# Optimization experiments

Hardware: AMD Instinct MI355X
Metric: run time of the kernel (lower is better)

## Reference

```python
import jax, jax.numpy as jnp
import numpy as np

B, S, E, H = 4, 2048, 1024, 16
D = E // H  # head_size = 64

def setup_inputs() -> dict:
    key = jax.random.key(0)
    ks = jax.random.split(key, 10)
    s_e = E ** -0.5
    s_4e = (4 * E) ** -0.5
    inp = {
        "x": jax.random.normal(ks[0], (B, S, E), dtype=jnp.float32),
        # per-head Q/K/V weights, stacked: [H, E, D], no bias
        "Wq": jax.random.normal(ks[1], (H, E, D), dtype=jnp.float32) * s_e,
        "Wk": jax.random.normal(ks[2], (H, E, D), dtype=jnp.float32) * s_e,
        "Wv": jax.random.normal(ks[3], (H, E, D), dtype=jnp.float32) * s_e,
        "Wo": jax.random.normal(ks[4], (E, E), dtype=jnp.float32) * s_e,
        "bo": jax.random.normal(ks[5], (E,), dtype=jnp.float32) * 0.01,
        "W1": jax.random.normal(ks[6], (E, 4 * E), dtype=jnp.float32) * s_e,
        "b1": jax.random.normal(ks[7], (4 * E,), dtype=jnp.float32) * 0.01,
        "W2": jax.random.normal(ks[8], (4 * E, E), dtype=jnp.float32) * s_4e,
        "b2": jax.random.normal(ks[9], (E,), dtype=jnp.float32) * 0.01,
    }
    return inp

def reference(x, Wq, Wk, Wv, Wo, bo, W1, b1, W2, b2):
    b, s, e = x.shape
    # NOTE: original scales by embedding_size**-0.5 (Size of x), not head_size
    scale = e ** -0.5
    q = jnp.einsum("bse,hed->bhsd", x, Wq)
    k = jnp.einsum("bse,hed->bhsd", x, Wk)
    v = jnp.einsum("bse,hed->bhsd", x, Wv)
    scores = jnp.einsum("bhsd,bhtd->bhst", q, k) * scale
    causal = jnp.tril(jnp.ones((s, s), dtype=bool))
    scores = jnp.where(causal, scores, -jnp.inf)
    weights = jax.nn.softmax(scores, axis=-1)
    attn = jnp.einsum("bhst,bhtd->bhsd", weights, v)  # [B,H,S,D]
    # concat heads along last dim: [B,S,H*D]
    attn = attn.transpose(0, 2, 1, 3).reshape(b, s, e)
    y = attn @ Wo + bo
    x = x + y  # residual (no LayerNorm applied in original forward)
    h = jax.nn.relu(x @ W1 + b1)
    ffn = h @ W2 + b2
    return x + ffn
```

## Files before the change

kernel.cpp:

```cpp
#include <hip/hip_runtime.h>
#include <stdint.h>

#define B_ 4
#define S_ 2048
#define E_ 1024
#define H_ 16
#define D_ 64

typedef unsigned short u16;
typedef u16 u16x8 __attribute__((ext_vector_type(8)));
typedef __bf16 bf16x8 __attribute__((ext_vector_type(8)));
typedef float f32x4 __attribute__((ext_vector_type(4)));

__device__ __forceinline__ float bf2f(u16 x) {
  unsigned int v = ((unsigned int)x) << 16;
  return __builtin_bit_cast(float, v);
}
__device__ __forceinline__ u16 f2bf(float f) {
  unsigned int u = __builtin_bit_cast(unsigned int, f);
  unsigned int r = (u + 0x7fffu + ((u >> 16) & 1u)) >> 16;
  return (u16)r;
}

__device__ __forceinline__ void gl2lds16(const u16* g, u16* l) {
  __builtin_amdgcn_global_load_lds(
      (const __attribute__((address_space(1))) void*)g,
      (__attribute__((address_space(3))) void*)l, 16, 0, 0);
}

__global__ __launch_bounds__(256) void cast_bf16_k(const float* __restrict__ src,
                                                   u16* __restrict__ dst, long n) {
  long i = ((long)blockIdx.x * 256 + threadIdx.x) * 8;
  if (i + 8 <= n) {
    f32x4 a = *(const f32x4*)(src + i), b = *(const f32x4*)(src + i + 4);
    u16x8 o;
#pragma unroll
    for (int j = 0; j < 4; j++) { o[j] = f2bf(a[j]); o[j + 4] = f2bf(b[j]); }
    *(u16x8*)(dst + i) = o;
  }
}

__global__ __launch_bounds__(256) void castT_k(const float* __restrict__ src,
                                               u16* __restrict__ dst, int R, int C) {
  long bofs = (long)blockIdx.z * R * C;
  src += bofs; dst += bofs;
  __shared__ u16 t[32][33];
  int c0 = blockIdx.x * 32, r0 = blockIdx.y * 32;
  int lc = threadIdx.x & 31, lr8 = threadIdx.x >> 5;
#pragma unroll
  for (int i = 0; i < 4; i++) {
    int lr = lr8 + i * 8;
    t[lr][lc] = f2bf(src[(long)(r0 + lr) * C + c0 + lc]);
  }
  __syncthreads();
#pragma unroll
  for (int i = 0; i < 4; i++) {
    int lr = lr8 + i * 8;
    dst[(long)(c0 + lr) * R + r0 + lc] = t[lc][lr];
  }
}

__global__ __launch_bounds__(256) void vT_k(const u16* __restrict__ QKV,
                                            u16* __restrict__ VTg) {
  int bh = blockIdx.z, d0 = blockIdx.y * 32, t0 = blockIdx.x * 32;
  int b = bh >> 4, h = bh & 15;
  __shared__ u16 t[32][33];
  int lc = threadIdx.x & 31, lr8 = threadIdx.x >> 5;
#pragma unroll
  for (int i = 0; i < 4; i++) {
    int lr = lr8 + i * 8;
    t[lr][lc] = QKV[(long)(b * S_ + t0 + lr) * 3072 + 2048 + h * 64 + d0 + lc];
  }
  __syncthreads();
#pragma unroll
  for (int i = 0; i < 4; i++) {
    int lr = lr8 + i * 8;
    VTg[((long)bh * 64 + d0 + lr) * S_ + t0 + lc] = t[lc][lr];
  }
}

template <bool AF32, bool CF32>
__global__ __launch_bounds__(256) void gemm128(const void* __restrict__ Av,
                                               const u16* __restrict__ BT,
                                               void* __restrict__ Cv,
                                               const float* __restrict__ bias,
                                               const float* __restrict__ resid,
                                               int M, int N, int K, int relu,
                                               u16* __restrict__ Cbf) {
  __shared__ u16 As[128 * 32];
  __shared__ u16 Bs[128 * 32];
  const int tid = threadIdx.x;
  const int wave = tid >> 6, lane = tid & 63;
  const int m0 = blockIdx.y * 128, n0 = blockIdx.x * 128;
  const int wm = wave >> 1, wn = wave & 1;
  const int fr = lane & 15, quad = lane >> 4;

  f32x4 acc[4][4] = {};

  const int srow = wave * 32 + (lane >> 2);
  const int skcol = (lane & 3) * 8;

  for (int k0 = 0; k0 < K; k0 += 32) {
    __syncthreads();
    if (AF32) {
      const float* Ap = (const float*)Av + (long)(m0 + (tid >> 1)) * K + k0 + (tid & 1) * 16;
      f32x4 f0 = *(const f32x4*)Ap, f1 = *(const f32x4*)(Ap + 4);
      f32x4 f2 = *(const f32x4*)(Ap + 8), f3 = *(const f32x4*)(Ap + 12);
      u16x8 p0, p1;
#pragma unroll
      for (int j = 0; j < 4; j++) {
        p0[j] = f2bf(f0[j]); p0[j + 4] = f2bf(f1[j]);
        p1[j] = f2bf(f2[j]); p1[j + 4] = f2bf(f3[j]);
      }
      *(u16x8*)&As[(tid >> 1) * 32 + (tid & 1) * 16] = p0;
      *(u16x8*)&As[(tid >> 1) * 32 + (tid & 1) * 16 + 8] = p1;
    } else {
      const u16* Ag = (const u16*)Av + (long)(m0 + srow) * K + k0 + skcol;
      gl2lds16(Ag, &As[(wave * 32) * 32]);
      gl2lds16(Ag + 16 * (long)K, &As[(wave * 32 + 16) * 32]);
    }
    {
      const u16* Bg = BT + (long)(n0 + srow) * K + k0 + skcol;
      gl2lds16(Bg, &Bs[(wave * 32) * 32]);
      gl2lds16(Bg + 16 * (long)K, &Bs[(wave * 32 + 16) * 32]);
    }
    __syncthreads();

    bf16x8 af[4], bfr[4];
#pragma unroll
    for (int mi = 0; mi < 4; mi++)
      af[mi] = __builtin_bit_cast(bf16x8, *(const u16x8*)&As[(wm * 64 + mi * 16 + fr) * 32 + quad * 8]);
#pragma unroll
    for (int ni = 0; ni < 4; ni++)
      bfr[ni] = __builtin_bit_cast(bf16x8, *(const u16x8*)&Bs[(wn * 64 + ni * 16 + fr) * 32 + quad * 8]);
#pragma unroll
    for (int mi = 0; mi < 4; mi++)
#pragma unroll
      for (int ni = 0; ni < 4; ni++)
        acc[mi][ni] = __builtin_amdgcn_mfma_f32_16x16x32_bf16(af[mi], bfr[ni], acc[mi][ni], 0, 0, 0);
  }

#pragma unroll
  for (int mi = 0; mi < 4; mi++)
#pragma unroll
    for (int ni = 0; ni < 4; ni++)
#pragma unroll
      for (int r = 0; r < 4; r++) {
        int gm = m0 + wm * 64 + mi * 16 + quad * 4 + r;
        int gn = n0 + wn * 64 + ni * 16 + fr;
        float v = acc[mi][ni][r];
        if (bias) v += bias[gn];
        if (resid) v += resid[(long)gm * N + gn];
        if (relu) v = fmaxf(v, 0.f);
        if (CF32) ((float*)Cv)[(long)gm * N + gn] = v;
        else      ((u16*)Cv)[(long)gm * N + gn] = f2bf(v);
        if (Cbf) Cbf[(long)gm * N + gn] = f2bf(v);
      }
}

__device__ __forceinline__ bf16x8 ldfrag32(const u16* base, int r, int quad) {
  int u = (r * 32 + quad * 8) ^ (((r >> 3) & 1) << 4);
  return __builtin_bit_cast(bf16x8, *(const u16x8*)(base + u));
}

__device__ __forceinline__ void stage_tile(const u16* __restrict__ A,
                                           const u16* __restrict__ BT, int K,
                                           int m0, int n0, int k0,
                                           u16* __restrict__ buf,
                                           int sr_, int sc_, int wbase) {
#pragma unroll
  for (int h = 0; h < 2; h++) {
    int r = h * 128 + sr_;
    int c = sc_ ^ (((r >> 3) & 1) << 4);
    gl2lds16(A + (size_t)(m0 + r) * K + k0 + c, buf + h * 4096 + wbase);
  }
  int c = sc_ ^ (((sr_ >> 3) & 1) << 4);
  gl2lds16(BT + (size_t)(n0 + sr_) * K + k0 + c, buf + 8192 + wbase);
}

template <bool CF32>
__global__ __launch_bounds__(512) void gemm3b(const u16* __restrict__ A,
                                              const u16* __restrict__ BT,
                                              void* __restrict__ Cv,
                                              const float* __restrict__ bias,
                                              const float* __restrict__ resid,
                                              int M, int N, int K, int relu,
                                              u16* __restrict__ Cbf) {
  (void)M;
  constexpr int BM = 256, BN = 128, BK = 32;
  constexpr int AU = BM * BK;
  constexpr int BUF = AU + BN * BK;

  __shared__ u16 sm[3 * BUF];
  const int tid = threadIdx.x;
  const int wave = tid >> 6, lane = tid & 63;
  const int wm = wave >> 1, wn = wave & 1;
  const int fr = lane & 15, quad = lane >> 4;

  const int nbx = gridDim.x;
  const int nwg = nbx * (int)gridDim.y;
  const int wgid = blockIdx.y * nbx + blockIdx.x;
  const int qq = nwg >> 3, rr = nwg & 7;
  const int xcd = wgid & 7, loc = wgid >> 3;
  const int sw = (xcd < rr ? xcd * (qq + 1) : rr * (qq + 1) + (xcd - rr) * qq) + loc;
  const int n0 = (sw % nbx) * BN;
  const int m0 = (sw / nbx) * BM;

  const int NT = K / BK;

  f32x4 acc[4][4] = {};

  const int sc_ = (tid & 3) * 8;
  const int sr_ = tid >> 2;
  const int wbase = wave << 9;

  const int rA = wm * 64 + fr;
  const int rB = wn * 64 + fr;

  stage_tile(A, BT, K, m0, n0, 0, sm, sr_, sc_, wbase);
  if (NT > 1) {
    stage_tile(A, BT, K, m0, n0, BK, sm + BUF, sr_, sc_, wbase);
    asm volatile("s_waitcnt vmcnt(3)" ::: "memory");
  } else {
    asm volatile("s_waitcnt vmcnt(0)" ::: "memory");
  }
  __builtin_amdgcn_s_barrier();

  int cur = 0;
  for (int t = 0; t < NT; ++t) {
    u16* cb = sm + cur * BUF;

    if (t + 2 < NT) {
      int s2 = cur + 2; if (s2 >= 3) s2 -= 3;
      stage_tile(A, BT, K, m0, n0, (t + 2) * BK, sm + s2 * BUF, sr_, sc_, wbase);
    }

    bf16x8 aF[4], bF[4];
#pragma unroll
    for (int mi = 0; mi < 4; ++mi) aF[mi] = ldfrag32(cb, rA + mi * 16, quad);
#pragma unroll
    for (int ni = 0; ni < 4; ++ni) bF[ni] = ldfrag32(cb + AU, rB + ni * 16, quad);

    asm volatile("s_waitcnt lgkmcnt(0)" ::: "memory");
    __builtin_amdgcn_sched_barrier(0);
    __builtin_amdgcn_s_setprio(1);
#pragma unroll
    for (int mi = 0; mi < 4; ++mi)
#pragma unroll
      for (int ni = 0; ni < 4; ++ni)
        acc[mi][ni] = __builtin_amdgcn_mfma_f32_16x16x32_bf16(aF[mi], bF[ni], acc[mi][ni], 0, 0, 0);
    __builtin_amdgcn_s_setprio(0);

    if (t + 2 < NT) asm volatile("s_waitcnt vmcnt(3)" ::: "memory");
    else            asm volatile("s_waitcnt vmcnt(0)" ::: "memory");
    __builtin_amdgcn_s_barrier();
    cur = cur + 1; if (cur >= 3) cur -= 3;
  }

#pragma unroll
  for (int mi = 0; mi < 4; ++mi)
#pragma unroll
    for (int ni = 0; ni < 4; ++ni)
#pragma unroll
      for (int r = 0; r < 4; ++r) {
        int gm = m0 + wm * 64 + mi * 16 + quad * 4 + r;
        int gn = n0 + wn * 64 + ni * 16 + fr;
        float v = acc[mi][ni][r];
        if (bias) v += bias[gn];
        if (resid) v += resid[(long)gm * N + gn];
        if (relu) v = fmaxf(v, 0.f);
        if (CF32) ((float*)Cv)[(long)gm * N + gn] = v;
        else      ((u16*)Cv)[(long)gm * N + gn] = f2bf(v);
        if (Cbf) Cbf[(long)gm * N + gn] = f2bf(v);
      }
}

__global__ __launch_bounds__(256) void attn_mfma4(const u16* __restrict__ QKV,
                                                  const u16* __restrict__ VTg,
                                                  u16* __restrict__ attn) {
  int p = blockIdx.x, h = blockIdx.y, b = blockIdx.z;
  int tid = threadIdx.x;
  int wq = tid >> 6, lane = tid & 63;
  int fr = lane & 15, quad = lane >> 4;
  int kf = quad * 8;

  __shared__ u16 Ks[2][64][72];
  __shared__ u16 Vt[2][64][72];
  __shared__ u16 QP[64 * 72];

  const u16* base = QKV + (long)b * S_ * 3072;
  const u16* vbase = VTg + (long)(b * 16 + h) * 64 * S_;
  int st = tid >> 2;
  int sd = (tid & 3) * 16;

  const float qsc = 0.03125f * 1.4426950408889634f;
  u16* Pw = QP + wq * (16 * 72);

  for (int ti = 0; ti < 2; ti++) {
    int qt = ti ? (31 - p) : p;

    __syncthreads();

    u16x8 ck0, ck1, cv0, cv1;
    {
      const u16* kr = base + (long)st * 3072 + 1024 + h * 64 + sd;
      ck0 = *(const u16x8*)kr; ck1 = *(const u16x8*)(kr + 8);
      const u16* vr = vbase + (long)st * S_ + sd;
      cv0 = *(const u16x8*)vr; cv1 = *(const u16x8*)(vr + 8);
    }

    {
      const u16* qr = base + (long)(qt * 64 + st) * 3072 + h * 64 + sd;
      u16x8 a = *(const u16x8*)qr, d = *(const u16x8*)(qr + 8);
      u16x8 oa, od;
#pragma unroll
      for (int j = 0; j < 8; j++) {
        oa[j] = f2bf(bf2f(a[j]) * qsc);
        od[j] = f2bf(bf2f(d[j]) * qsc);
      }
      *(u16x8*)&QP[st * 72 + sd] = oa;
      *(u16x8*)&QP[st * 72 + sd + 8] = od;
    }
    __syncthreads();
    bf16x8 qf0 = __builtin_bit_cast(bf16x8, *(const u16x8*)&QP[(wq * 16 + fr) * 72 + kf]);
    bf16x8 qf1 = __builtin_bit_cast(bf16x8, *(const u16x8*)&QP[(wq * 16 + fr) * 72 + 32 + kf]);

    f32x4 acc[4] = {};
    float l[4] = {0.f, 0.f, 0.f, 0.f};

    for (int c = 0; c <= qt; c++) {
      int bi = c & 1;
      *(u16x8*)&Ks[bi][st][sd] = ck0;
      *(u16x8*)&Ks[bi][st][sd + 8] = ck1;
      *(u16x8*)&Vt[bi][st][sd] = cv0;
      *(u16x8*)&Vt[bi][st][sd + 8] = cv1;
      if (c < qt) {
        int t0n = (c + 1) * 64;
        const u16* kr = base + (long)(t0n + st) * 3072 + 1024 + h * 64 + sd;
        ck0 = *(const u16x8*)kr; ck1 = *(const u16x8*)(kr + 8);
        const u16* vr = vbase + (long)st * S_ + t0n + sd;
        cv0 = *(const u16x8*)vr; cv1 = *(const u16x8*)(vr + 8);
      }
      __syncthreads();

      f32x4 sc[4] = {};
#pragma unroll
      for (int nt = 0; nt < 4; nt++) {
        bf16x8 b0 = __builtin_bit_cast(bf16x8, *(const u16x8*)&Ks[bi][nt * 16 + fr][kf]);
        bf16x8 b1 = __builtin_bit_cast(bf16x8, *(const u16x8*)&Ks[bi][nt * 16 + fr][32 + kf]);
        sc[nt] = __builtin_amdgcn_mfma_f32_16x16x32_bf16(qf0, b0, sc[nt], 0, 0, 0);
        sc[nt] = __builtin_amdgcn_mfma_f32_16x16x32_bf16(qf1, b1, sc[nt], 0, 0, 0);
      }

      if (c == qt) {
        int qloc = wq * 16 + quad * 4;
#pragma unroll
        for (int nt = 0; nt < 4; nt++)
#pragma unroll
          for (int r = 0; r < 4; r++)
            if (nt * 16 + fr > qloc + r) sc[nt][r] = -1e30f;
      }

      const int prow = quad * 4;
#pragma unroll
      for (int nt = 0; nt < 4; nt++) {
        int col = nt * 16 + fr;
#pragma unroll
        for (int r = 0; r < 4; r++) {
          float pv = exp2f(sc[nt][r]);
          l[r] += pv;
          Pw[(prow + r) * 72 + col] = f2bf(pv);
        }
      }

      bf16x8 pa0 = __builtin_bit_cast(bf16x8, *(const u16x8*)&Pw[fr * 72 + kf]);
      bf16x8 pa1 = __builtin_bit_cast(bf16x8, *(const u16x8*)&Pw[fr * 72 + 32 + kf]);
#pragma unroll
      for (int nt = 0; nt < 4; nt++) {
        bf16x8 vb0 = __builtin_bit_cast(bf16x8, *(const u16x8*)&Vt[bi][nt * 16 + fr][kf]);
        bf16x8 vb1 = __builtin_bit_cast(bf16x8, *(const u16x8*)&Vt[bi][nt * 16 + fr][32 + kf]);
        acc[nt] = __builtin_amdgcn_mfma_f32_16x16x32_bf16(pa0, vb0, acc[nt], 0, 0, 0);
        acc[nt] = __builtin_amdgcn_mfma_f32_16x16x32_bf16(pa1, vb1, acc[nt], 0, 0, 0);
      }
    }

#pragma unroll
    for (int r = 0; r < 4; r++)
#pragma unroll
      for (int off = 1; off < 16; off <<= 1) l[r] += __shfl_xor(l[r], off);

    long row = (long)b * S_ + qt * 64 + wq * 16 + quad * 4;
#pragma unroll
    for (int nt = 0; nt < 4; nt++)
#pragma unroll
      for (int r = 0; r < 4; r++)
        attn[(row + r) * 1024 + h * 64 + nt * 16 + fr] = f2bf(acc[nt][r] / l[r]);
  }
}

extern "C" void kernel_launch(void* const* d_in, const int* in_sizes, int n_in,
                              void* d_out, int out_size, void* d_ws, size_t ws_size,
                              hipStream_t stream) {
  (void)in_sizes; (void)n_in; (void)out_size;
  const float* x  = (const float*)d_in[0];
  const float* Wq = (const float*)d_in[1];
  const float* Wk = (const float*)d_in[2];
  const float* Wv = (const float*)d_in[3];
  const float* Wo = (const float*)d_in[4];
  const float* bo = (const float*)d_in[5];
  const float* W1 = (const float*)d_in[6];
  const float* b1 = (const float*)d_in[7];
  const float* W2 = (const float*)d_in[8];
  const float* b2 = (const float*)d_in[9];
  float* out = (float*)d_out;

  char* ws = (char*)d_ws;
  u16*   QKV  = (u16*)(ws);
  u16*   attn = (u16*)(ws + 50331648);
  u16*   hbuf = (u16*)(ws);
  float* x1   = (float*)(ws + 67108864);
  u16*   VTg  = (u16*)(ws + 67108864);
  u16*   xb   = (u16*)(ws + 83886080);
  u16*   WT   = (u16*)(ws + 100663296);
  u16*   WoT  = (u16*)(ws + 106954752);
  u16*   W1T  = (u16*)(ws + 109051904);
  u16*   W2T  = (u16*)(ws + 117440512);
  u16*   x1b  = (u16*)(ws + 125829120);
  bool bigws = ws_size >= (size_t)142606336;

  cast_bf16_k<<<4096, 256, 0, stream>>>(x, xb, (long)8192 * 1024);
  castT_k<<<dim3(2, 32, 16), 256, 0, stream>>>(Wq, WT, 1024, 64);
  castT_k<<<dim3(2, 32, 16), 256, 0, stream>>>(Wk, WT + 1048576, 1024, 64);
  castT_k<<<dim3(2, 32, 16), 256, 0, stream>>>(Wv, WT + 2097152, 1024, 64);
  castT_k<<<dim3(32, 32, 1), 256, 0, stream>>>(Wo, WoT, 1024, 1024);
  castT_k<<<dim3(128, 32, 1), 256, 0, stream>>>(W1, W1T, 1024, 4096);
  castT_k<<<dim3(32, 128, 1), 256, 0, stream>>>(W2, W2T, 4096, 1024);

  gemm3b<false><<<dim3(24, 32), 512, 0, stream>>>(xb, WT, QKV, nullptr, nullptr, 8192, 3072, 1024, 0, nullptr);
  vT_k<<<dim3(64, 2, 64), 256, 0, stream>>>(QKV, VTg);
  attn_mfma4<<<dim3(16, H_, B_), 256, 0, stream>>>(QKV, VTg, attn);
  gemm3b<true><<<dim3(8, 32), 512, 0, stream>>>(attn, WoT, x1, bo, x, 8192, 1024, 1024, 0, bigws ? x1b : nullptr);
  if (bigws)
    gemm3b<false><<<dim3(32, 32), 512, 0, stream>>>(x1b, W1T, hbuf, b1, nullptr, 8192, 4096, 1024, 1, nullptr);
  else
    gemm128<true, false><<<dim3(32, 64), 256, 0, stream>>>(x1, W1T, hbuf, b1, nullptr, 8192, 4096, 1024, 1, nullptr);
  gemm3b<true><<<dim3(8, 32), 512, 0, stream>>>(hbuf, W2T, out, b2, x1, 8192, 1024, 4096, 0, nullptr);
}
```

Before: 538.8 us.

## Process 128-query blocks with 8 waves sharing each staged K/V chunk

The attention kernel drops the two-tile balanced loop (tile p and tile 31-p) and gives each block 128 contiguous query rows, handled by 8 waves of 512 threads. Every K/V chunk staged in LDS is now read by twice as many waves, which halves global-to-LDS traffic per query. Load balance is lost: block qb does qb*2+2 chunks, so causal work is no longer paired and later blocks run longer. Waves whose rows are already past the diagonal sit idle through the final chunk while still joining the barriers.

```diff
diff --git a/kernel.cpp b/kernel.cpp
--- a/kernel.cpp
+++ b/kernel.cpp
@@ -275,10 +275,10 @@
       }
 }
 
-__global__ __launch_bounds__(256) void attn_mfma4(const u16* __restrict__ QKV,
+__global__ __launch_bounds__(512) void attn_mfma5(const u16* __restrict__ QKV,
                                                   const u16* __restrict__ VTg,
                                                   u16* __restrict__ attn) {
-  int p = blockIdx.x, h = blockIdx.y, b = blockIdx.z;
+  int qb = blockIdx.x, h = blockIdx.y, b = blockIdx.z;
   int tid = threadIdx.x;
   int wq = tid >> 6, lane = tid & 63;
   int fr = lane & 15, quad = lane >> 4;
@@ -286,63 +286,61 @@
 
   __shared__ u16 Ks[2][64][72];
   __shared__ u16 Vt[2][64][72];
-  __shared__ u16 QP[64 * 72];
+  __shared__ u16 QP[128 * 72];
 
   const u16* base = QKV + (long)b * S_ * 3072;
   const u16* vbase = VTg + (long)(b * 16 + h) * 64 * S_;
-  int st = tid >> 2;
-  int sd = (tid & 3) * 16;
+
+  const int stK = tid >> 3;
+  const int sdK = (tid & 7) * 8;
+  const int stQ = tid >> 2;
+  const int sdQ = (tid & 3) * 16;
 
   const float qsc = 0.03125f * 1.4426950408889634f;
   u16* Pw = QP + wq * (16 * 72);
 
-  for (int ti = 0; ti < 2; ti++) {
-    int qt = ti ? (31 - p) : p;
-
+  const int nch = qb * 2 + 2;
+  const int wlast = qb * 2 + (wq >> 2);
+
+  u16x8 ck, cv;
+  {
+    const u16* kr = base + (long)stK * 3072 + 1024 + h * 64 + sdK;
+    ck = *(const u16x8*)kr;
+    const u16* vr = vbase + (long)stK * S_ + sdK;
+    cv = *(const u16x8*)vr;
+  }
+
+  {
+    const u16* qr = base + (long)(qb * 128 + stQ) * 3072 + h * 64 + sdQ;
+    u16x8 a = *(const u16x8*)qr, d = *(const u16x8*)(qr + 8);
+    u16x8 oa, od;
+#pragma unroll
+    for (int j = 0; j < 8; j++) {
+      oa[j] = f2bf(bf2f(a[j]) * qsc);
+      od[j] = f2bf(bf2f(d[j]) * qsc);
+    }
+    *(u16x8*)&QP[stQ * 72 + sdQ] = oa;
+    *(u16x8*)&QP[stQ * 72 + sdQ + 8] = od;
+  }
+  __syncthreads();
+  bf16x8 qf0 = __builtin_bit_cast(bf16x8, *(const u16x8*)&QP[(wq * 16 + fr) * 72 + kf]);
+  bf16x8 qf1 = __builtin_bit_cast(bf16x8, *(const u16x8*)&QP[(wq * 16 + fr) * 72 + 32 + kf]);
+
+  f32x4 acc[4] = {};
+  float l[4] = {0.f, 0.f, 0.f, 0.f};
+
+  for (int c = 0; c < nch; c++) {
+    int bi = c & 1;
+    *(u16x8*)&Ks[bi][stK][sdK] = ck;
+    *(u16x8*)&Vt[bi][stK][sdK] = cv;
+    if (c + 1 < nch) {
+      int t0n = (c + 1) * 64;
+      ck = *(const u16x8*)(base + (long)(t0n + stK) * 3072 + 1024 + h * 64 + sdK);
+      cv = *(const u16x8*)(vbase + (long)stK * S_ + t0n + sdK);
+    }
     __syncthreads();
 
-    u16x8 ck0, ck1, cv0, cv1;
-    {
-      const u16* kr = base + (long)st * 3072 + 1024 + h * 64 + sd;
-      ck0 = *(const u16x8*)kr; ck1 = *(const u16x8*)(kr + 8);
-      const u16* vr = vbase + (long)st * S_ + sd;
-      cv0 = *(const u16x8*)vr; cv1 = *(const u16x8*)(vr + 8);
-    }
-
-    {
-      const u16* qr = base + (long)(qt * 64 + st) * 3072 + h * 64 + sd;
-      u16x8 a = *(const u16x8*)qr, d = *(const u16x8*)(qr + 8);
-      u16x8 oa, od;
-#pragma unroll
-      for (int j = 0; j < 8; j++) {
-        oa[j] = f2bf(bf2f(a[j]) * qsc);
-        od[j] = f2bf(bf2f(d[j]) * qsc);
-      }
-      *(u16x8*)&QP[st * 72 + sd] = oa;
-      *(u16x8*)&QP[st * 72 + sd + 8] = od;
-    }
-    __syncthreads();
-    bf16x8 qf0 = __builtin_bit_cast(bf16x8, *(const u16x8*)&QP[(wq * 16 + fr) * 72 + kf]);
-    bf16x8 qf1 = __builtin_bit_cast(bf16x8, *(const u16x8*)&QP[(wq * 16 + fr) * 72 + 32 + kf]);
-
-    f32x4 acc[4] = {};
-    float l[4] = {0.f, 0.f, 0.f, 0.f};
-
-    for (int c = 0; c <= qt; c++) {
-      int bi = c & 1;
-      *(u16x8*)&Ks[bi][st][sd] = ck0;
-      *(u16x8*)&Ks[bi][st][sd + 8] = ck1;
-      *(u16x8*)&Vt[bi][st][sd] = cv0;
-      *(u16x8*)&Vt[bi][st][sd + 8] = cv1;
-      if (c < qt) {
-        int t0n = (c + 1) * 64;
-        const u16* kr = base + (long)(t0n + st) * 3072 + 1024 + h * 64 + sd;
-        ck0 = *(const u16x8*)kr; ck1 = *(const u16x8*)(kr + 8);
-        const u16* vr = vbase + (long)st * S_ + t0n + sd;
-        cv0 = *(const u16x8*)vr; cv1 = *(const u16x8*)(vr + 8);
-      }
-      __syncthreads();
-
+    if (c <= wlast) {
       f32x4 sc[4] = {};
 #pragma unroll
       for (int nt = 0; nt < 4; nt++) {
@@ -352,8 +350,8 @@
         sc[nt] = __builtin_amdgcn_mfma_f32_16x16x32_bf16(qf1, b1, sc[nt], 0, 0, 0);
       }
 
-      if (c == qt) {
-        int qloc = wq * 16 + quad * 4;
+      if (c == wlast) {
+        int qloc = (wq & 3) * 16 + quad * 4;
 #pragma unroll
         for (int nt = 0; nt < 4; nt++)
 #pragma unroll
@@ -383,19 +381,19 @@
         acc[nt] = __builtin_amdgcn_mfma_f32_16x16x32_bf16(pa1, vb1, acc[nt], 0, 0, 0);
       }
     }
-
+  }
+
+#pragma unroll
+  for (int r = 0; r < 4; r++)
+#pragma unroll
+    for (int off = 1; off < 16; off <<= 1) l[r] += __shfl_xor(l[r], off);
+
+  long row = (long)b * S_ + qb * 128 + wq * 16 + quad * 4;
+#pragma unroll
+  for (int nt = 0; nt < 4; nt++)
 #pragma unroll
     for (int r = 0; r < 4; r++)
-#pragma unroll
-      for (int off = 1; off < 16; off <<= 1) l[r] += __shfl_xor(l[r], off);
-
-    long row = (long)b * S_ + qt * 64 + wq * 16 + quad * 4;
-#pragma unroll
-    for (int nt = 0; nt < 4; nt++)
-#pragma unroll
-      for (int r = 0; r < 4; r++)
-        attn[(row + r) * 1024 + h * 64 + nt * 16 + fr] = f2bf(acc[nt][r] / l[r]);
-  }
+      attn[(row + r) * 1024 + h * 64 + nt * 16 + fr] = f2bf(acc[nt][r] / l[r]);
 }
 
 extern "C" void kernel_launch(void* const* d_in, const int* in_sizes, int n_in,
@@ -438,7 +436,7 @@
 
   gemm3b<false><<<dim3(24, 32), 512, 0, stream>>>(xb, WT, QKV, nullptr, nullptr, 8192, 3072, 1024, 0, nullptr);
   vT_k<<<dim3(64, 2, 64), 256, 0, stream>>>(QKV, VTg);
-  attn_mfma4<<<dim3(16, H_, B_), 256, 0, stream>>>(QKV, VTg, attn);
+  attn_mfma5<<<dim3(16, H_, B_), 512, 0, stream>>>(QKV, VTg, attn);
   gemm3b<true><<<dim3(8, 32), 512, 0, stream>>>(attn, WoT, x1, bo, x, 8192, 1024, 1024, 0, bigws ? x1b : nullptr);
   if (bigws)
     gemm3b<false><<<dim3(32, 32), 512, 0, stream>>>(x1b, W1T, hbuf, b1, nullptr, 8192, 4096, 1024, 1, nullptr);
```

After: 578.4 us. 7.3% more time.

## Process both paired query tiles in one pass over shared K/V chunks

Applied to the files above, without the earlier changes.

The attention kernel previously processed its two causal-balanced query tiles (p and 31-p) sequentially, reloading K/V chunks for each. Now both tiles' Q fragments are kept in registers and a single loop over K/V chunks serves both, skipping the low tile once past its diagonal. This removes the duplicate K/V global loads and LDS staging for the shorter tile, at the cost of more registers for the doubled accumulators and a larger LDS Q/P buffer, which may reduce occupancy.

```diff
diff --git a/kernel.cpp b/kernel.cpp
--- a/kernel.cpp
+++ b/kernel.cpp
@@ -275,7 +275,7 @@
       }
 }
 
-__global__ __launch_bounds__(256) void attn_mfma4(const u16* __restrict__ QKV,
+__global__ __launch_bounds__(256) void attn_mfma6(const u16* __restrict__ QKV,
                                                   const u16* __restrict__ VTg,
                                                   u16* __restrict__ attn) {
   int p = blockIdx.x, h = blockIdx.y, b = blockIdx.z;
@@ -286,7 +286,7 @@
 
   __shared__ u16 Ks[2][64][72];
   __shared__ u16 Vt[2][64][72];
-  __shared__ u16 QP[64 * 72];
+  __shared__ u16 QP[128 * 72];
 
   const u16* base = QKV + (long)b * S_ * 3072;
   const u16* vbase = VTg + (long)(b * 16 + h) * 64 * S_;
@@ -294,62 +294,70 @@
   int sd = (tid & 3) * 16;
 
   const float qsc = 0.03125f * 1.4426950408889634f;
-  u16* Pw = QP + wq * (16 * 72);
-
-  for (int ti = 0; ti < 2; ti++) {
-    int qt = ti ? (31 - p) : p;
-
+
+  const int qlo = p, qhi = 31 - p;
+  const int nch = qhi + 1;
+
+  u16x8 ck0, ck1, cv0, cv1;
+  {
+    const u16* kr = base + (long)st * 3072 + 1024 + h * 64 + sd;
+    ck0 = *(const u16x8*)kr; ck1 = *(const u16x8*)(kr + 8);
+    const u16* vr = vbase + (long)st * S_ + sd;
+    cv0 = *(const u16x8*)vr; cv1 = *(const u16x8*)(vr + 8);
+  }
+
+#pragma unroll
+  for (int t2 = 0; t2 < 2; t2++) {
+    int qrow = (t2 ? qhi : qlo) * 64 + st;
+    const u16* qr = base + (long)qrow * 3072 + h * 64 + sd;
+    u16x8 a = *(const u16x8*)qr, d = *(const u16x8*)(qr + 8);
+    u16x8 oa, od;
+#pragma unroll
+    for (int j = 0; j < 8; j++) {
+      oa[j] = f2bf(bf2f(a[j]) * qsc);
+      od[j] = f2bf(bf2f(d[j]) * qsc);
+    }
+    *(u16x8*)&QP[(t2 * 64 + st) * 72 + sd] = oa;
+    *(u16x8*)&QP[(t2 * 64 + st) * 72 + sd + 8] = od;
+  }
+  __syncthreads();
+  bf16x8 qf[2][2];
+#pragma unroll
+  for (int t = 0; t < 2; t++) {
+    qf[t][0] = __builtin_bit_cast(bf16x8, *(const u16x8*)&QP[(t * 64 + wq * 16 + fr) * 72 + kf]);
+    qf[t][1] = __builtin_bit_cast(bf16x8, *(const u16x8*)&QP[(t * 64 + wq * 16 + fr) * 72 + 32 + kf]);
+  }
+
+  f32x4 acc[2][4] = {};
+  float l[2][4] = {};
+
+  for (int c = 0; c < nch; c++) {
+    int bi = c & 1;
+    *(u16x8*)&Ks[bi][st][sd] = ck0;
+    *(u16x8*)&Ks[bi][st][sd + 8] = ck1;
+    *(u16x8*)&Vt[bi][st][sd] = cv0;
+    *(u16x8*)&Vt[bi][st][sd + 8] = cv1;
+    if (c + 1 < nch) {
+      int t0n = (c + 1) * 64;
+      const u16* kr = base + (long)(t0n + st) * 3072 + 1024 + h * 64 + sd;
+      ck0 = *(const u16x8*)kr; ck1 = *(const u16x8*)(kr + 8);
+      const u16* vr = vbase + (long)st * S_ + t0n + sd;
+      cv0 = *(const u16x8*)vr; cv1 = *(const u16x8*)(vr + 8);
+    }
     __syncthreads();
 
-    u16x8 ck0, ck1, cv0, cv1;
-    {
-      const u16* kr = base + (long)st * 3072 + 1024 + h * 64 + sd;
-      ck0 = *(const u16x8*)kr; ck1 = *(const u16x8*)(kr + 8);
-      const u16* vr = vbase + (long)st * S_ + sd;
-      cv0 = *(const u16x8*)vr; cv1 = *(const u16x8*)(vr + 8);
-    }
-
-    {
-      const u16* qr = base + (long)(qt * 64 + st) * 3072 + h * 64 + sd;
-      u16x8 a = *(const u16x8*)qr, d = *(const u16x8*)(qr + 8);
-      u16x8 oa, od;
-#pragma unroll
-      for (int j = 0; j < 8; j++) {
-        oa[j] = f2bf(bf2f(a[j]) * qsc);
-        od[j] = f2bf(bf2f(d[j]) * qsc);
-      }
-      *(u16x8*)&QP[st * 72 + sd] = oa;
-      *(u16x8*)&QP[st * 72 + sd + 8] = od;
-    }
-    __syncthreads();
-    bf16x8 qf0 = __builtin_bit_cast(bf16x8, *(const u16x8*)&QP[(wq * 16 + fr) * 72 + kf]);
-    bf16x8 qf1 = __builtin_bit_cast(bf16x8, *(const u16x8*)&QP[(wq * 16 + fr) * 72 + 32 + kf]);
-
-    f32x4 acc[4] = {};
-    float l[4] = {0.f, 0.f, 0.f, 0.f};
-
-    for (int c = 0; c <= qt; c++) {
-      int bi = c & 1;
-      *(u16x8*)&Ks[bi][st][sd] = ck0;
-      *(u16x8*)&Ks[bi][st][sd + 8] = ck1;
-      *(u16x8*)&Vt[bi][st][sd] = cv0;
-      *(u16x8*)&Vt[bi][st][sd + 8] = cv1;
-      if (c < qt) {
-        int t0n = (c + 1) * 64;
-        const u16* kr = base + (long)(t0n + st) * 3072 + 1024 + h * 64 + sd;
-        ck0 = *(const u16x8*)kr; ck1 = *(const u16x8*)(kr + 8);
-        const u16* vr = vbase + (long)st * S_ + t0n + sd;
-        cv0 = *(const u16x8*)vr; cv1 = *(const u16x8*)(vr + 8);
-      }
-      __syncthreads();
+#pragma unroll
+    for (int t = 0; t < 2; t++) {
+      int qt = t ? qhi : qlo;
+      if (t == 0 && c > qlo) continue;
 
       f32x4 sc[4] = {};
 #pragma unroll
       for (int nt = 0; nt < 4; nt++) {
         bf16x8 b0 = __builtin_bit_cast(bf16x8, *(const u16x8*)&Ks[bi][nt * 16 + fr][kf]);
         bf16x8 b1 = __builtin_bit_cast(bf16x8, *(const u16x8*)&Ks[bi][nt * 16 + fr][32 + kf]);
-        sc[nt] = __builtin_amdgcn_mfma_f32_16x16x32_bf16(qf0, b0, sc[nt], 0, 0, 0);
-        sc[nt] = __builtin_amdgcn_mfma_f32_16x16x32_bf16(qf1, b1, sc[nt], 0, 0, 0);
+        sc[nt] = __builtin_amdgcn_mfma_f32_16x16x32_bf16(qf[t][0], b0, sc[nt], 0, 0, 0);
+        sc[nt] = __builtin_amdgcn_mfma_f32_16x16x32_bf16(qf[t][1], b1, sc[nt], 0, 0, 0);
       }
 
       if (c == qt) {
@@ -361,6 +369,7 @@
             if (nt * 16 + fr > qloc + r) sc[nt][r] = -1e30f;
       }
 
+      u16* Pw = QP + (t * 64 + wq * 16) * 72;
       const int prow = quad * 4;
 #pragma unroll
       for (int nt = 0; nt < 4; nt++) {
@@ -368,7 +377,7 @@
 #pragma unroll
         for (int r = 0; r < 4; r++) {
           float pv = exp2f(sc[nt][r]);
-          l[r] += pv;
+          l[t][r] += pv;
           Pw[(prow + r) * 72 + col] = f2bf(pv);
         }
       }
@@ -379,22 +388,25 @@
       for (int nt = 0; nt < 4; nt++) {
         bf16x8 vb0 = __builtin_bit_cast(bf16x8, *(const u16x8*)&Vt[bi][nt * 16 + fr][kf]);
         bf16x8 vb1 = __builtin_bit_cast(bf16x8, *(const u16x8*)&Vt[bi][nt * 16 + fr][32 + kf]);
-        acc[nt] = __builtin_amdgcn_mfma_f32_16x16x32_bf16(pa0, vb0, acc[nt], 0, 0, 0);
-        acc[nt] = __builtin_amdgcn_mfma_f32_16x16x32_bf16(pa1, vb1, acc[nt], 0, 0, 0);
-      }
-    }
-
+        acc[t][nt] = __builtin_amdgcn_mfma_f32_16x16x32_bf16(pa0, vb0, acc[t][nt], 0, 0, 0);
+        acc[t][nt] = __builtin_amdgcn_mfma_f32_16x16x32_bf16(pa1, vb1, acc[t][nt], 0, 0, 0);
+      }
+    }
+  }
+
+#pragma unroll
+  for (int t = 0; t < 2; t++) {
 #pragma unroll
     for (int r = 0; r < 4; r++)
 #pragma unroll
-      for (int off = 1; off < 16; off <<= 1) l[r] += __shfl_xor(l[r], off);
-
-    long row = (long)b * S_ + qt * 64 + wq * 16 + quad * 4;
+      for (int off = 1; off < 16; off <<= 1) l[t][r] += __shfl_xor(l[t][r], off);
+
+    long row = (long)b * S_ + (long)(t ? qhi : qlo) * 64 + wq * 16 + quad * 4;
 #pragma unroll
     for (int nt = 0; nt < 4; nt++)
 #pragma unroll
       for (int r = 0; r < 4; r++)
-        attn[(row + r) * 1024 + h * 64 + nt * 16 + fr] = f2bf(acc[nt][r] / l[r]);
+        attn[(row + r) * 1024 + h * 64 + nt * 16 + fr] = f2bf(acc[t][nt][r] / l[t][r]);
   }
 }
 
@@ -438,7 +450,7 @@
 
   gemm3b<false><<<dim3(24, 32), 512, 0, stream>>>(xb, WT, QKV, nullptr, nullptr, 8192, 3072, 1024, 0, nullptr);
   vT_k<<<dim3(64, 2, 64), 256, 0, stream>>>(QKV, VTg);
-  attn_mfma4<<<dim3(16, H_, B_), 256, 0, stream>>>(QKV, VTg, attn);
+  attn_mfma6<<<dim3(16, H_, B_), 256, 0, stream>>>(QKV, VTg, attn);
   gemm3b<true><<<dim3(8, 32), 512, 0, stream>>>(attn, WoT, x1, bo, x, 8192, 1024, 1024, 0, bigws ? x1b : nullptr);
   if (bigws)
     gemm3b<false><<<dim3(32, 32), 512, 0, stream>>>(x1b, W1T, hbuf, b1, nullptr, 8192, 4096, 1024, 1, nullptr);
```

Result: slower. 568.8 us (+5.6%).
